# Kernel optimization log

Measured on AMD Instinct MI355X. Metric: run time of the kernel, lower is better.

Reference implementation:

```python
import jax, jax.numpy as jnp
import numpy as np

QMAX = 127.0

def setup_inputs() -> dict:
    key = jax.random.key(0)
    kx, kw, ks = jax.random.split(key, 3)
    B, S, D_IN, D_OUT = 4, 2048, 4096, 4096
    x = jax.random.normal(kx, (B, S, D_IN), dtype=jnp.float16)
    # int8 weight buffer, same distribution as torch.randint(-127, 127)
    weight = jax.random.randint(kw, (D_OUT, D_IN), -127, 127, dtype=jnp.int32).astype(jnp.int8)
    # per-output-channel weight scales (fp16 buffer); small positive values
    weight_scales = (jax.random.uniform(ks, (D_OUT,), dtype=jnp.float32) * 0.01 + 1e-4).astype(jnp.float16)
    return {"x": x, "weight": weight, "weight_scales": weight_scales}

def reference(x, weight, weight_scales):
    # x: [B, S, D_in] fp16; weight: [D_out, D_in] int8; weight_scales: [D_out] fp16
    x32 = x.astype(jnp.float32)
    # dynamic per-token absmax quantization: scale = absmax / 127
    absmax = jnp.max(jnp.abs(x32), axis=-1, keepdims=True)      # [B, S, 1]
    x_scales = jnp.maximum(absmax / QMAX, 1e-8)
    q = jnp.round(x32 / x_scales)                                # in [-127, 127]
    q = jnp.clip(q, -QMAX, QMAX).astype(jnp.int8)
    # int8 GEMM accumulated in int32 (cupy.matmul on int32 in the original)
    y = jnp.einsum('bsk,nk->bsn', q.astype(jnp.int32), weight.astype(jnp.int32),
                   preferred_element_type=jnp.int32)             # [B, S, D_out]
    # dequant: per-token activation scale * per-channel weight scale
    y = y.astype(jnp.float32) * x_scales * weight_scales.astype(jnp.float32)[None, None, :]
    return y.astype(jnp.float16)
```

## Files before the change

### kernel.cpp

```cpp
#include <hip/hip_runtime.h>
#include <stdint.h>

typedef int int32x4 __attribute__((ext_vector_type(4)));

constexpr int K_DIM = 4096;
constexpr int N_DIM = 4096;
constexpr float QMAXF = 127.0f;

__global__ __launch_bounds__(256) void quant_rows(const float* __restrict__ x,
                                                  int8_t* __restrict__ q,
                                                  float* __restrict__ scales) {
    const int row = blockIdx.x;
    const int tid = threadIdx.x;
    const size_t base = (size_t)row * K_DIM;

    const float4* xv = reinterpret_cast<const float4*>(x + base);
    float4 v[4];
#pragma unroll
    for (int i = 0; i < 4; ++i) v[i] = xv[tid + 256 * i];

    float m = 0.0f;
#pragma unroll
    for (int i = 0; i < 4; ++i)
        m = fmaxf(m, fmaxf(fmaxf(fabsf(v[i].x), fabsf(v[i].y)),
                           fmaxf(fabsf(v[i].z), fabsf(v[i].w))));
#pragma unroll
    for (int off = 32; off > 0; off >>= 1) m = fmaxf(m, __shfl_xor(m, off));

    __shared__ float wmax[4];
    if ((tid & 63) == 0) wmax[tid >> 6] = m;
    __syncthreads();
    const float am = fmaxf(fmaxf(wmax[0], wmax[1]), fmaxf(wmax[2], wmax[3]));
    const float scale = fmaxf(am * (1.0f / 127.0f), 1e-8f);
    if (tid == 0) scales[row] = scale;
    const float inv = 1.0f / scale;

    int* qw = reinterpret_cast<int*>(q + base);
#pragma unroll
    for (int i = 0; i < 4; ++i) {
        float f0 = fminf(QMAXF, fmaxf(-QMAXF, rintf(v[i].x * inv)));
        float f1 = fminf(QMAXF, fmaxf(-QMAXF, rintf(v[i].y * inv)));
        float f2 = fminf(QMAXF, fmaxf(-QMAXF, rintf(v[i].z * inv)));
        float f3 = fminf(QMAXF, fmaxf(-QMAXF, rintf(v[i].w * inv)));
        int b0 = ((int)f0) & 255, b1 = ((int)f1) & 255;
        int b2 = ((int)f2) & 255, b3 = ((int)f3) & 255;
        qw[tid + 256 * i] = b0 | (b1 << 8) | (b2 << 16) | (b3 << 24);
    }
}

__global__ __launch_bounds__(256) void pack_w(const int* __restrict__ w,
                                              int8_t* __restrict__ w8) {
    const int idx = blockIdx.x * 256 + threadIdx.x;
    const int4 v = reinterpret_cast<const int4*>(w)[idx];
    int packed = (v.x & 255) | ((v.y & 255) << 8) | ((v.z & 255) << 16) | ((v.w & 255) << 24);
    reinterpret_cast<int*>(w8)[idx] = packed;
}

constexpr int BM = 256, BN = 256, BK = 64;
constexpr int NT = K_DIM / BK;

#define GLL(src, dst)                                                          \
    __builtin_amdgcn_global_load_lds(                                          \
        (const __attribute__((address_space(1))) unsigned int*)(src),          \
        (__attribute__((address_space(3))) unsigned int*)(dst), 16, 0, 0)

#define MFMA_I8(a, b, c) __builtin_amdgcn_mfma_i32_16x16x64_i8((a), (b), (c), 0, 0, 0)

__global__ __launch_bounds__(512, 2) void w8a8_gemm256(
        const int8_t* __restrict__ A, const int8_t* __restrict__ B,
        const float* __restrict__ asc, const float* __restrict__ wsc,
        float* __restrict__ C, int M) {
    extern __shared__ int8_t lds[];

    const int tid  = threadIdx.x;
    const int lane = tid & 63;
    const int wave = tid >> 6;

    const int nwg = gridDim.x;
    const int bid = blockIdx.x;
    const int swz = (bid & 7) * (nwg >> 3) + (bid >> 3);
    const int NB  = N_DIM / BN;
    const int brow = (swz / NB) * BM;
    const int bcol = (swz % NB) * BN;

    const int wm = wave >> 2;
    const int wn = wave & 3;
    const int l15 = lane & 15;
    const int ls  = lane >> 4;

    const int s0 = tid, s1 = tid + 512;
    const int r0s = s0 >> 2, g0 = (s0 & 3) ^ ((s0 >> 3) & 3);
    const int r1s = s1 >> 2, g1 = (s1 & 3) ^ ((s1 >> 3) & 3);
    const int8_t* gA0 = A + (size_t)(brow + r0s) * K_DIM + g0 * 16;
    const int8_t* gA1 = A + (size_t)(brow + r1s) * K_DIM + g1 * 16;
    const int8_t* gB0 = B + (size_t)(bcol + r0s) * K_DIM + g0 * 16;
    const int8_t* gB1 = B + (size_t)(bcol + r1s) * K_DIM + g1 * 16;
    const int segb0 = wave * 1024;
    const int segb1 = segb0 + 8192;

    const int gsz  = ls ^ ((l15 >> 1) & 3);
    const int offA = (wm * 128 + l15) * BK + gsz * 16;
    const int offB = (wn * 64  + l15) * BK + gsz * 16;

    int32x4 acc[8][4];
#pragma unroll
    for (int i = 0; i < 8; ++i)
#pragma unroll
        for (int j = 0; j < 4; ++j) acc[i][j] = (int32x4){0, 0, 0, 0};

#pragma unroll
    for (int tt = 0; tt < 3; ++tt) {
        GLL(gA0 + tt * BK, lds + tt * 16384 + segb0);
        GLL(gA1 + tt * BK, lds + tt * 16384 + segb1);
        GLL(gB0 + tt * BK, lds + 65536 + tt * 16384 + segb0);
        GLL(gB1 + tt * BK, lds + 65536 + tt * 16384 + segb1);
    }
    asm volatile("s_waitcnt vmcnt(8)" ::: "memory");
    __builtin_amdgcn_s_barrier();

    for (int t = 0; t < NT; ++t) {
        const int8_t* Ab = lds + (t & 3) * 16384;
        const int8_t* Bb = lds + 65536 + (t & 3) * 16384;
        int8_t* dA = lds + ((t + 3) & 3) * 16384;
        int8_t* dB = lds + 65536 + ((t + 3) & 3) * 16384;
        const bool pf = (t + 3 < NT);
        const int kk = (t + 3) * BK;

        int32x4 af[4], bf[4];

        if (pf) {
            GLL(gA0 + kk, dA + segb0);
            GLL(gA1 + kk, dA + segb1);
        }
#pragma unroll
        for (int mi = 0; mi < 4; ++mi)
            af[mi] = *(const int32x4*)(Ab + offA + mi * 1024);
#pragma unroll
        for (int ni = 0; ni < 4; ++ni)
            bf[ni] = *(const int32x4*)(Bb + offB + ni * 1024);
        __builtin_amdgcn_s_barrier();
        asm volatile("s_waitcnt lgkmcnt(0)" ::: "memory");
        __builtin_amdgcn_sched_barrier(0);
        __builtin_amdgcn_s_setprio(1);
#pragma unroll
        for (int mi = 0; mi < 4; ++mi)
#pragma unroll
            for (int ni = 0; ni < 4; ++ni)
                acc[mi][ni] = MFMA_I8(af[mi], bf[ni], acc[mi][ni]);
        __builtin_amdgcn_s_setprio(0);
        __builtin_amdgcn_s_barrier();

        if (pf) {
            GLL(gB0 + kk, dB + segb0);
            GLL(gB1 + kk, dB + segb1);
        }
#pragma unroll
        for (int mi = 0; mi < 4; ++mi)
            af[mi] = *(const int32x4*)(Ab + offA + (mi + 4) * 1024);
        __builtin_amdgcn_s_barrier();
        asm volatile("s_waitcnt lgkmcnt(0)" ::: "memory");
        __builtin_amdgcn_sched_barrier(0);
        __builtin_amdgcn_s_setprio(1);
#pragma unroll
        for (int mi = 0; mi < 4; ++mi)
#pragma unroll
            for (int ni = 0; ni < 4; ++ni)
                acc[mi + 4][ni] = MFMA_I8(af[mi], bf[ni], acc[mi + 4][ni]);
        __builtin_amdgcn_s_setprio(0);
        if (t <= NT - 4)      asm volatile("s_waitcnt vmcnt(8)" ::: "memory");
        else if (t == NT - 3) asm volatile("s_waitcnt vmcnt(4)" ::: "memory");
        else                  asm volatile("s_waitcnt vmcnt(0)" ::: "memory");
        __builtin_amdgcn_sched_barrier(0);
        __builtin_amdgcn_s_barrier();
    }

    const int c0  = lane & 15;
    const int rr0 = (lane >> 4) * 4;
#pragma unroll
    for (int ni = 0; ni < 4; ++ni) {
        const int col = bcol + wn * 64 + ni * 16 + c0;
        const float ws = wsc[col];
#pragma unroll
        for (int mi = 0; mi < 8; ++mi) {
            const int rowb = brow + wm * 128 + mi * 16 + rr0;
#pragma unroll
            for (int r = 0; r < 4; ++r) {
                const int row = rowb + r;
                float o = (float)acc[mi][ni][r] * asc[row] * ws;
                o = (float)(_Float16)o;
                C[(size_t)row * N_DIM + col] = o;
            }
        }
    }
}

extern "C" void kernel_launch(void* const* d_in, const int* in_sizes, int n_in,
                              void* d_out, int out_size, void* d_ws, size_t ws_size,
                              hipStream_t stream) {
    const float* x   = (const float*)d_in[0];
    const int*   w   = (const int*)d_in[1];
    const float* wsc = (const float*)d_in[2];
    float* out = (float*)d_out;

    const int K = K_DIM;
    const int M = in_sizes[0] / K;
    const int N = N_DIM;

    int8_t* q   = (int8_t*)d_ws;
    int8_t* w8  = (int8_t*)d_ws + (size_t)M * K;
    float*  asc = (float*)((char*)d_ws + (size_t)M * K + (size_t)N * K);

    quant_rows<<<M, 256, 0, stream>>>(x, q, asc);
    pack_w<<<(N * (K / 4)) / 256, 256, 0, stream>>>(w, w8);
    const int grid = (M / BM) * (N / BN);
    w8a8_gemm256<<<grid, 512, 131072, stream>>>(q, w8, asc, wsc, out, M);
}
```

Measured before the change: 200.5 us.

## Shrink GEMM tile to 256x128 with 4 waves and 3-stage single-barrier pipeline

Reworks the int8 GEMM from a 256x256 tile with 8 waves and a 4-deep LDS ring into a 256x128 tile with 4 waves and a 3-deep ring. Each wave now computes a 128x64 sub-tile in one pass per K step, with a single barrier per iteration instead of the split half-step schedule. LDS use drops to 72KB, so more workgroups can be resident per CU and the grid doubles. The cost is lower arithmetic intensity per tile, which means more global and LDS traffic per MFMA, and a shallower prefetch depth.

```diff
diff --git a/kernel.cpp b/kernel.cpp
--- a/kernel.cpp
+++ b/kernel.cpp
@@ -56,8 +56,11 @@
     reinterpret_cast<int*>(w8)[idx] = packed;
 }
 
-constexpr int BM = 256, BN = 256, BK = 64;
+constexpr int BM = 256, BN = 128, BK = 64;
 constexpr int NT = K_DIM / BK;
+constexpr int A_RING = 16384;
+constexpr int B_RING = 8192;
+constexpr int B_BASE = 3 * A_RING;
 
 #define GLL(src, dst)                                                          \
     __builtin_amdgcn_global_load_lds(                                          \
@@ -66,7 +69,7 @@
 
 #define MFMA_I8(a, b, c) __builtin_amdgcn_mfma_i32_16x16x64_i8((a), (b), (c), 0, 0, 0)
 
-__global__ __launch_bounds__(512, 2) void w8a8_gemm256(
+__global__ __launch_bounds__(256, 2) void w8a8_gemm(
         const int8_t* __restrict__ A, const int8_t* __restrict__ B,
         const float* __restrict__ asc, const float* __restrict__ wsc,
         float* __restrict__ C, int M) {
@@ -79,24 +82,20 @@
     const int nwg = gridDim.x;
     const int bid = blockIdx.x;
     const int swz = (bid & 7) * (nwg >> 3) + (bid >> 3);
-    const int NB  = N_DIM / BN;
-    const int brow = (swz / NB) * BM;
-    const int bcol = (swz % NB) * BN;
-
-    const int wm = wave >> 2;
-    const int wn = wave & 3;
+    const int brow = (swz >> 5) * BM;
+    const int bcol = (swz & 31) * BN;
+
+    const int wm = wave >> 1;
+    const int wn = wave & 1;
     const int l15 = lane & 15;
     const int ls  = lane >> 4;
 
-    const int s0 = tid, s1 = tid + 512;
-    const int r0s = s0 >> 2, g0 = (s0 & 3) ^ ((s0 >> 3) & 3);
-    const int r1s = s1 >> 2, g1 = (s1 & 3) ^ ((s1 >> 3) & 3);
-    const int8_t* gA0 = A + (size_t)(brow + r0s) * K_DIM + g0 * 16;
-    const int8_t* gA1 = A + (size_t)(brow + r1s) * K_DIM + g1 * 16;
-    const int8_t* gB0 = B + (size_t)(bcol + r0s) * K_DIM + g0 * 16;
-    const int8_t* gB1 = B + (size_t)(bcol + r1s) * K_DIM + g1 * 16;
-    const int segb0 = wave * 1024;
-    const int segb1 = segb0 + 8192;
+    const int rowst = tid >> 2;
+    const int g     = (tid & 3) ^ ((tid >> 3) & 3);
+    const int8_t* gA = A + (size_t)(brow + rowst) * K_DIM + g * 16;
+    const int8_t* gB = B + (size_t)(bcol + rowst) * K_DIM + g * 16;
+    const size_t chunk_g = (size_t)64 * K_DIM;
+    const int wbase = wave * 1024;
 
     const int gsz  = ls ^ ((l15 >> 1) & 3);
     const int offA = (wm * 128 + l15) * BK + gsz * 16;
@@ -109,67 +108,53 @@
         for (int j = 0; j < 4; ++j) acc[i][j] = (int32x4){0, 0, 0, 0};
 
 #pragma unroll
-    for (int tt = 0; tt < 3; ++tt) {
-        GLL(gA0 + tt * BK, lds + tt * 16384 + segb0);
-        GLL(gA1 + tt * BK, lds + tt * 16384 + segb1);
-        GLL(gB0 + tt * BK, lds + 65536 + tt * 16384 + segb0);
-        GLL(gB1 + tt * BK, lds + 65536 + tt * 16384 + segb1);
-    }
-    asm volatile("s_waitcnt vmcnt(8)" ::: "memory");
+    for (int tt = 0; tt < 2; ++tt) {
+#pragma unroll
+        for (int c = 0; c < 4; ++c)
+            GLL(gA + tt * BK + c * chunk_g, lds + tt * A_RING + c * 4096 + wbase);
+#pragma unroll
+        for (int c = 0; c < 2; ++c)
+            GLL(gB + tt * BK + c * chunk_g, lds + B_BASE + tt * B_RING + c * 4096 + wbase);
+    }
+    asm volatile("s_waitcnt vmcnt(6)" ::: "memory");
     __builtin_amdgcn_s_barrier();
 
     for (int t = 0; t < NT; ++t) {
-        const int8_t* Ab = lds + (t & 3) * 16384;
-        const int8_t* Bb = lds + 65536 + (t & 3) * 16384;
-        int8_t* dA = lds + ((t + 3) & 3) * 16384;
-        int8_t* dB = lds + 65536 + ((t + 3) & 3) * 16384;
-        const bool pf = (t + 3 < NT);
-        const int kk = (t + 3) * BK;
-
-        int32x4 af[4], bf[4];
-
-        if (pf) {
-            GLL(gA0 + kk, dA + segb0);
-            GLL(gA1 + kk, dA + segb1);
+        const int cs = t % 3;
+        const int8_t* Ab = lds + cs * A_RING;
+        const int8_t* Bb = lds + B_BASE + cs * B_RING;
+
+        if (t < NT - 2) {
+            const int ps = (t + 2) % 3;
+            const int kk = (t + 2) * BK;
+#pragma unroll
+            for (int c = 0; c < 4; ++c)
+                GLL(gA + kk + c * chunk_g, lds + ps * A_RING + c * 4096 + wbase);
+#pragma unroll
+            for (int c = 0; c < 2; ++c)
+                GLL(gB + kk + c * chunk_g, lds + B_BASE + ps * B_RING + c * 4096 + wbase);
         }
-#pragma unroll
-        for (int mi = 0; mi < 4; ++mi)
+
+        int32x4 af[8], bf[4];
+#pragma unroll
+        for (int mi = 0; mi < 8; ++mi)
             af[mi] = *(const int32x4*)(Ab + offA + mi * 1024);
 #pragma unroll
         for (int ni = 0; ni < 4; ++ni)
             bf[ni] = *(const int32x4*)(Bb + offB + ni * 1024);
-        __builtin_amdgcn_s_barrier();
+
         asm volatile("s_waitcnt lgkmcnt(0)" ::: "memory");
         __builtin_amdgcn_sched_barrier(0);
         __builtin_amdgcn_s_setprio(1);
 #pragma unroll
-        for (int mi = 0; mi < 4; ++mi)
+        for (int mi = 0; mi < 8; ++mi)
 #pragma unroll
             for (int ni = 0; ni < 4; ++ni)
                 acc[mi][ni] = MFMA_I8(af[mi], bf[ni], acc[mi][ni]);
         __builtin_amdgcn_s_setprio(0);
-        __builtin_amdgcn_s_barrier();
-
-        if (pf) {
-            GLL(gB0 + kk, dB + segb0);
-            GLL(gB1 + kk, dB + segb1);
-        }
-#pragma unroll
-        for (int mi = 0; mi < 4; ++mi)
-            af[mi] = *(const int32x4*)(Ab + offA + (mi + 4) * 1024);
-        __builtin_amdgcn_s_barrier();
-        asm volatile("s_waitcnt lgkmcnt(0)" ::: "memory");
-        __builtin_amdgcn_sched_barrier(0);
-        __builtin_amdgcn_s_setprio(1);
-#pragma unroll
-        for (int mi = 0; mi < 4; ++mi)
-#pragma unroll
-            for (int ni = 0; ni < 4; ++ni)
-                acc[mi + 4][ni] = MFMA_I8(af[mi], bf[ni], acc[mi + 4][ni]);
-        __builtin_amdgcn_s_setprio(0);
-        if (t <= NT - 4)      asm volatile("s_waitcnt vmcnt(8)" ::: "memory");
-        else if (t == NT - 3) asm volatile("s_waitcnt vmcnt(4)" ::: "memory");
-        else                  asm volatile("s_waitcnt vmcnt(0)" ::: "memory");
+
+        if (t < NT - 2)       asm volatile("s_waitcnt vmcnt(6)" ::: "memory");
+        else if (t == NT - 2) asm volatile("s_waitcnt vmcnt(0)" ::: "memory");
         __builtin_amdgcn_sched_barrier(0);
         __builtin_amdgcn_s_barrier();
     }
@@ -213,5 +198,5 @@
     quant_rows<<<M, 256, 0, stream>>>(x, q, asc);
     pack_w<<<(N * (K / 4)) / 256, 256, 0, stream>>>(w, w8);
     const int grid = (M / BM) * (N / BN);
-    w8a8_gemm256<<<grid, 512, 131072, stream>>>(q, w8, asc, wsc, out, M);
-}
+    w8a8_gemm<<<grid, 256, 73728, stream>>>(q, w8, asc, wsc, out, M);
+}
```

Result: no change. 200.1 us (-0.2%).
